# Kernel optimization log

Hardware: AMD Instinct MI355X
Metric: run time of the kernel (lower is better)

The kernel has to match this reference:

```python
import jax, jax.numpy as jnp
import numpy as np

H, D, VD = 8, 64, 64
QD, KD, VDIM, OUT = 512, 512, 512, 512
N, QS, VS = 16, 512, 512
TEMP = 10.0              # softstair_temp
SCALING = D ** -0.5


def _softstair(x):
    fl = jnp.floor(x)
    return fl + jax.nn.sigmoid(TEMP * (jnp.abs(x - fl) - 0.5))


def setup_inputs() -> dict:
    key = jax.random.key(0)
    ks = jax.random.split(key, 24)
    f = jax.random.normal
    s = 0.03  # xavier-ish scale
    return {
        "Q": f(ks[0], (N, QS, QD), jnp.float32),
        "K": f(ks[1], (N, VS, KD), jnp.float32),
        "V": f(ks[2], (N, VS, VDIM), jnp.float32),
        "past_state": f(ks[3], (N, H, QS, D), jnp.float32),
        "past_attention": jax.random.uniform(ks[4], (N, H, QS, 1), jnp.float32),
        "value_positions": jnp.arange(VS, dtype=jnp.float32),
        "attention_mask": jnp.ones((N, QS, VS), jnp.int32),
        "Wq": f(ks[5], (QD, H * D), jnp.float32) * s,
        "Wk": f(ks[6], (KD, H * D), jnp.float32) * s,
        "Wv": f(ks[7], (VDIM, H * VD), jnp.float32) * s,
        "Wpos": f(ks[8], (QD, H * D), jnp.float32) * s,
        "bpos": f(ks[9], (H * D,), jnp.float32) * s,
        "Wsigma": f(ks[10], (H, D, 1), jnp.float32) * s,
        "Wrho": f(ks[11], (H, D, 3), jnp.float32) * s,
        "mix_w": f(ks[12], (QD, 1), jnp.float32) * s,
        "mix_b": f(ks[13], (1,), jnp.float32) * s,
        "gru_wi": f(ks[14], (D, 3 * D), jnp.float32) * s,
        "gru_wh": f(ks[15], (D, 3 * D), jnp.float32) * s,
        "gru_bi": f(ks[16], (3 * D,), jnp.float32) * s,
        "gru_bh": f(ks[17], (3 * D,), jnp.float32) * s,
        "Wc": f(ks[18], (H * VD, OUT), jnp.float32) * s,
    }


def reference(Q, K, V, past_state, past_attention, value_positions, attention_mask,
              Wq, Wk, Wv, Wpos, bpos, Wsigma, Wrho, mix_w, mix_b,
              gru_wi, gru_wh, gru_bi, gru_bh, Wc):
    n, qS, _ = Q.shape
    vS = K.shape[1]
    mask_f = attention_mask.astype(jnp.float32)          # [N,qS,vS]
    mask_b = attention_mask.astype(bool)[:, None]        # [N,1,qS,vS]
    lengths = jnp.sum(mask_f, axis=-1)                   # [N,qS]
    l_1 = jnp.maximum(1.0, lengths - 1.0)[:, None, :, None]
    step_size = 1.0 / l_1                                # [N,1,qS,1]
    nvp = value_positions[None, None, None, :] * step_size  # [N,1,qS,vS]

    # mix gate
    mix = jax.nn.sigmoid(Q @ mix_w + mix_b)[:, None]     # [N,1,qS,1]

    # projections -> [N,H,S,d]
    Qpos = (Q @ Wpos + bpos).reshape(n, qS, H, D).transpose(0, 2, 1, 3)
    Qh = (Q @ Wq).reshape(n, qS, H, D).transpose(0, 2, 1, 3)
    Kh = (K @ Wk).reshape(n, vS, H, D).transpose(0, 2, 1, 3)
    Vh = (V @ Wv).reshape(n, vS, H, VD).transpose(0, 2, 1, 3)

    # content attention
    content = jnp.einsum('bhqd,bhkd->bhqk', Qh, Kh) * SCALING
    content_attn = jax.nn.softmax(jnp.where(mask_b, content, -jnp.inf), axis=-1)

    # GRUCell update (torch gate order r,z,n) on relu(Qpos) with past_state
    x = jax.nn.relu(Qpos)
    gi = x @ gru_wi + gru_bi
    gh = past_state @ gru_wh + gru_bh
    ir, iz, inn = jnp.split(gi, 3, axis=-1)
    hr, hz, hn = jnp.split(gh, 3, axis=-1)
    r = jax.nn.sigmoid(ir + hr)
    z = jax.nn.sigmoid(iz + hz)
    nn_ = jnp.tanh(inn + r * hn)
    state = (1.0 - z) * nn_ + z * past_state             # [N,H,qS,D]

    # location (Gaussian) attention
    sigma = (jax.nn.relu(jnp.einsum('bhqd,hde->bhqe', state, Wsigma)) + 0.27) \
            / lengths[:, None, :, None]                  # [N,H,qS,1]
    rho = jnp.einsum('bhqd,hde->bhqe', state, Wrho)      # [N,H,qS,3]
    steps = _softstair(rho[..., 0:1])
    attn_gate = jax.nn.sigmoid(rho[..., 1:2])
    bias_gate = jax.nn.sigmoid(rho[..., 2:3])
    mu_ = steps * step_size + attn_gate * past_attention + bias_gate
    # leaky clamp to [0,1]
    mu = jnp.maximum(0.01 * mu_, jnp.minimum(mu_, 1.0 + 0.01 * mu_))
    diff = nvp - mu                                      # [N,H,qS,vS]
    gauss = jnp.exp(-(diff * diff) / (2.0 * sigma * sigma))
    g = gauss * mask_f[:, None]
    pos_attn = g / jnp.sum(g + 1e-20, axis=-1, keepdims=True)

    scores = mix * pos_attn + (1.0 - mix) * content_attn
    attended = jnp.einsum('bhqk,bhkv->bhqv', scores, Vh)
    out = attended.transpose(0, 2, 1, 3).reshape(n, qS, H * VD) @ Wc
    return out
```

## Files before the change

kernel.cpp:

```cpp
#include <hip/hip_runtime.h>


typedef __bf16 bf16;
typedef __bf16 bfx8 __attribute__((ext_vector_type(8)));
typedef float v4f __attribute__((ext_vector_type(4)));

__device__ inline float sigm(float x) { return 1.0f / (1.0f + __expf(-x)); }
__device__ inline float tanh_fast(float x) { return 1.0f - 2.0f / (__expf(2.0f * x) + 1.0f); }

__device__ inline v4f mfma16(bfx8 a, bfx8 b, v4f c) {
    return __builtin_amdgcn_mfma_f32_16x16x32_bf16(a, b, c, 0, 0, 0);
}

typedef const __attribute__((address_space(1))) void* gvp;
typedef __attribute__((address_space(3))) void* lvp;

__device__ inline void gload_lds16(const bf16* g, bf16* l) {
    __builtin_amdgcn_global_load_lds((gvp)g, (lvp)l, 16, 0, 0);
}

__device__ inline void split8(const float* __restrict__ p, bfx8& hi, bfx8& lo) {
    float4 x = *(const float4*)p;
    float4 y = *(const float4*)(p + 4);
    float v[8] = {x.x, x.y, x.z, x.w, y.x, y.y, y.z, y.w};
#pragma unroll
    for (int j = 0; j < 8; ++j) {
        bf16 h = (bf16)v[j];
        hi[j] = h;
        lo[j] = (bf16)(v[j] - (float)h);
    }
}

struct PrepArgs {
    const float* wsrc[5]; bf16* wdst[5]; bf16* wdstlo[5];
    const float* gwi; const float* gwh;
    bf16* wih; bf16* wil; bf16* whh; bf16* whl;
    const float* Q; const int* mask; const float* mix_w; const float* mix_b;
    float* mixv; float* stepv; float* lenv; unsigned* mpack;
    const float* Kf; const float* Vf;
    bf16* Qbf; bf16* Qlo; bf16* Kbf; bf16* Vbf;
};

__global__ __launch_bounds__(256) void prep_kernel(PrepArgs a) {
    __shared__ __align__(16) char smraw[17408];
    const int b = blockIdx.x;
    const int t = threadIdx.x;

    if (b < 320) {
        float (*tile)[68] = (float(*)[68])smraw;
        const int wy = b >> 6, bx = b & 63;
        const float* src = a.wsrc[wy];
        bf16* dst = a.wdst[wy];
        bf16* dlo = a.wdstlo[wy];
        const int rbase = (bx >> 3) * 64, cbase = (bx & 7) * 64;
        const int r = t >> 2, cc = (t & 3) * 16;
        {
            const float* p = src + (long)(rbase + r) * 512 + cbase + cc;
            *(float4*)(&tile[r][cc]) = *(const float4*)p;
            *(float4*)(&tile[r][cc + 4]) = *(const float4*)(p + 4);
            *(float4*)(&tile[r][cc + 8]) = *(const float4*)(p + 8);
            *(float4*)(&tile[r][cc + 12]) = *(const float4*)(p + 12);
        }
        __syncthreads();
        bfx8 h0, h1, l0, l1;
#pragma unroll
        for (int j = 0; j < 8; ++j) {
            float v0 = tile[cc + j][r];
            float v1 = tile[cc + 8 + j][r];
            bf16 a0 = (bf16)v0, a1 = (bf16)v1;
            h0[j] = a0; l0[j] = (bf16)(v0 - (float)a0);
            h1[j] = a1; l1[j] = (bf16)(v1 - (float)a1);
        }
        const int n_ = cbase + r;
        const int x_ = (n_ & 7) << 3;
        const long rowo = (long)n_ * 512;
        const int ka = (rbase + cc) ^ x_;
        const int kb = (rbase + cc + 8) ^ x_;
        *(bfx8*)(dst + rowo + ka) = h0;
        *(bfx8*)(dst + rowo + kb) = h1;
        if (dlo) {
            *(bfx8*)(dlo + rowo + ka) = l0;
            *(bfx8*)(dlo + rowo + kb) = l1;
        }
        return;
    }

    if (b < 322) {
        const int m = b - 320;
        const float* src = m ? a.gwh : a.gwi;
        bf16* dh = m ? a.whh : a.wih;
        bf16* dl = m ? a.whl : a.wil;
        for (int e = t; e < 12288; e += 256) {
            int n_ = e >> 6, k = e & 63;
            float v = src[k * 192 + n_];
            bf16 h = (bf16)v;
            dh[e] = h;
            dl[e] = (bf16)(v - (float)h);
        }
        return;
    }

    if (b < 834) {
        unsigned (*mwords)[16] = (unsigned(*)[16])smraw;
        const int bm = b - 322;
        const int qt = bm & 31, n = bm >> 5;
        const int wave = t >> 6, lane = t & 63;
#pragma unroll
        for (int rr = 0; rr < 4; ++rr) {
            const int rloc = wave * 4 + rr;
            const long row = (long)n * 512 + qt * 16 + rloc;
            float dot = 0.f, ms = 0.f;
            unsigned myw = 0;
#pragma unroll
            for (int j = 0; j < 8; ++j) {
                float qv = a.Q[row * 512 + j * 64 + lane];
                float wv = a.mix_w[j * 64 + lane];
                dot += qv * wv;
                int mv = a.mask[row * 512 + j * 64 + lane];
                unsigned long long bl = __ballot(mv != 0);
                ms += (float)__popcll(bl);
                if ((lane >> 1) == j) myw = (unsigned)(bl >> ((lane & 1) * 32));
            }
#pragma unroll
            for (int o = 32; o > 0; o >>= 1) dot += __shfl_xor(dot, o);
            if (lane < 16) mwords[rloc][lane] = myw;
            if (lane == 0) {
                a.mixv[row] = sigm(dot + a.mix_b[0]);
                a.lenv[row] = ms;
                a.stepv[row] = 1.0f / fmaxf(1.0f, ms - 1.0f);
            }
        }
        __syncthreads();
        {
            const int quad = (lane >> 4), c = lane & 15;
            unsigned out = 0;
#pragma unroll
            for (int i = 0; i < 4; ++i) {
                const int rl = quad * 4 + i;
                unsigned w0 = mwords[rl][wave * 4 + 0];
                unsigned w1 = mwords[rl][wave * 4 + 1];
                unsigned w2 = mwords[rl][wave * 4 + 2];
                unsigned w3 = mwords[rl][wave * 4 + 3];
                unsigned byte_ = ((w0 >> c) & 1u) | (((w0 >> (16 + c)) & 1u) << 1) |
                                 (((w1 >> c) & 1u) << 2) | (((w1 >> (16 + c)) & 1u) << 3) |
                                 (((w2 >> c) & 1u) << 4) | (((w2 >> (16 + c)) & 1u) << 5) |
                                 (((w3 >> c) & 1u) << 6) | (((w3 >> (16 + c)) & 1u) << 7);
                out |= byte_ << (8 * i);
            }
            a.mpack[(long)bm * 256 + t] = out;
        }
        return;
    }

    const int cb = b - 834;
    const int tensor = cb >> 10;
    const long off = ((long)(cb & 1023) * 256 + t) * 16;
    const float* s_ = tensor == 0 ? a.Q : (tensor == 1 ? a.Kf : a.Vf);
    const float4* sp = (const float4*)(s_ + off);
    float4 x0 = sp[0], x1 = sp[1], x2 = sp[2], x3 = sp[3];
    float v[16] = {x0.x, x0.y, x0.z, x0.w, x1.x, x1.y, x1.z, x1.w,
                   x2.x, x2.y, x2.z, x2.w, x3.x, x3.y, x3.z, x3.w};
    bfx8 h0, h1, l0, l1;
#pragma unroll
    for (int j = 0; j < 8; ++j) {
        bf16 ha = (bf16)v[j], hb = (bf16)v[8 + j];
        h0[j] = ha; h1[j] = hb;
        l0[j] = (bf16)(v[j] - (float)ha);
        l1[j] = (bf16)(v[8 + j] - (float)hb);
    }
    bf16* dh = tensor == 0 ? a.Qbf : (tensor == 1 ? a.Kbf : a.Vbf);
    *(bfx8*)(dh + off) = h0;
    *(bfx8*)(dh + off + 8) = h1;
    if (tensor == 0) {
        *(bfx8*)(a.Qlo + off) = l0;
        *(bfx8*)(a.Qlo + off + 8) = l1;
    }
}

struct GEMMDesc {
    const bf16* A0;
    const bf16* A1;
    const bf16* B0;
    const bf16* B1;
    const float* bias;
    bf16* Cb;
    bf16* Cl;
    float* Cf;
    int mode;
    float cscale;
};
struct G4 { GEMMDesc d[4]; };

__global__ __launch_bounds__(256, 3) void gemm128(G4 gg) {
    __shared__ bf16 sm[16384];
    bf16* Bs0 = sm;
    bf16* Bs1 = sm + 8192;

    const GEMMDesc g = gg.d[blockIdx.z];
    const int mode = g.mode;
    const int mbase = blockIdx.x * 128, nbase = blockIdx.y * 128;
    const int t = threadIdx.x, w = t >> 6, l = t & 63;
    const int quad = l >> 4, c = l & 15;
    const int wr = w >> 1, wc = w & 1;

    const v4f zero4 = {0.f, 0.f, 0.f, 0.f};
    v4f acc[4][4];
#pragma unroll
    for (int m = 0; m < 4; ++m)
#pragma unroll
        for (int nn = 0; nn < 4; ++nn) acc[m][nn] = zero4;

    const int nsteps = (mode == 2) ? 24 : 8;
    const int xm = c & 7;
    const int slot0 = w * 4;
    const int srow = l >> 3;
    const int sch8 = (l & 7) * 8;
    const long arow = (long)(mbase + wr * 64 + c) * 512 + quad * 8;

    auto issueB = [&](int s, bf16* Bs) {
        const bf16* Bsrc = (mode == 2 && ((s >> 3) == 1)) ? g.B1 : g.B0;
        const int k0 = (mode == 2) ? (s & 7) * 64 : s * 64;
#pragma unroll
        for (int j = 0; j < 4; ++j) {
            int sl = slot0 + j;
            int row = sl * 8 + srow;
            gload_lds16(Bsrc + (long)(nbase + row) * 512 + k0 + sch8, Bs + sl * 512);
        }
    };

    auto loadA = [&](int s, bfx8 (&dst)[8]) {
        const bf16* Asrc = (mode == 2 && ((s >> 3) == 2)) ? g.A1 : g.A0;
        const int k0 = (mode == 2) ? (s & 7) * 64 : s * 64;
#pragma unroll
        for (int m = 0; m < 4; ++m) {
            const bf16* pr = Asrc + arow + (long)m * 16 * 512 + k0;
            dst[m * 2 + 0] = *(const bfx8*)pr;
            dst[m * 2 + 1] = *(const bfx8*)(pr + 32);
        }
    };

    auto computeB = [&](const bf16* Bs, const bfx8 (&af)[8]) {
#pragma unroll
        for (int ks = 0; ks < 2; ++ks) {
            const int off = (((ks * 4 + quad) ^ xm) * 8);
            bfx8 bb[4];
#pragma unroll
            for (int nn = 0; nn < 4; ++nn)
                bb[nn] = *(const bfx8*)(&Bs[(wc * 64 + nn * 16 + c) * 64 + off]);
#pragma unroll
            for (int m = 0; m < 4; ++m)
#pragma unroll
                for (int nn = 0; nn < 4; ++nn)
                    acc[m][nn] = mfma16(af[m * 2 + ks], bb[nn], acc[m][nn]);
        }
    };

    bfx8 aA[8], aB[8];
    issueB(0, Bs0);
    loadA(0, aA);
    __syncthreads();
    for (int s = 0; s < nsteps; s += 2) {
        issueB(s + 1, Bs1);
        loadA(s + 1, aB);
        computeB(Bs0, aA);
        __syncthreads();
        const bool more = (s + 2 < nsteps);
        if (more) {
            issueB(s + 2, Bs0);
            loadA(s + 2, aA);
        }
        computeB(Bs1, aB);
        __syncthreads();
    }

    if (mode == 3) {
        float* C = g.Cf;
#pragma unroll
        for (int m = 0; m < 4; ++m)
#pragma unroll
            for (int nn = 0; nn < 4; ++nn)
#pragma unroll
                for (int i = 0; i < 4; ++i) {
                    int row = mbase + wr * 64 + m * 16 + quad * 4 + i;
                    int col = nbase + wc * 64 + nn * 16 + c;
                    C[(long)row * 512 + col] = acc[m][nn][i];
                }
        return;
    }

    if (mode == 1) {
        bf16* CT = g.Cb + ((long)(mbase >> 9)) * 262144;
        const int s0 = mbase & 511;
        for (int h = 0; h < 2; ++h) {
            if (wr == h) {
#pragma unroll
                for (int m = 0; m < 4; ++m)
#pragma unroll
                    for (int nn = 0; nn < 4; ++nn)
#pragma unroll
                        for (int i = 0; i < 4; ++i)
                            sm[(wc * 64 + nn * 16 + c) * 64 + m * 16 + quad * 4 + i] =
                                (bf16)acc[m][nn][i];
            }
            __syncthreads();
            {
                const bf16* src = sm + (t >> 1) * 64 + (t & 1) * 32;
                bf16* d = CT + (long)(nbase + (t >> 1)) * 512 + s0 + h * 64 + (t & 1) * 32;
#pragma unroll
                for (int j = 0; j < 4; ++j) *(bfx8*)(d + j * 8) = *(const bfx8*)(src + j * 8);
            }
            __syncthreads();
        }
        return;
    }

    for (int h = 0; h < 2; ++h) {
        if (wr == h) {
#pragma unroll
            for (int m = 0; m < 4; ++m)
#pragma unroll
                for (int nn = 0; nn < 4; ++nn)
#pragma unroll
                    for (int i = 0; i < 4; ++i) {
                        int col = wc * 64 + nn * 16 + c;
                        float v = acc[m][nn][i];
                        if (mode == 2) v = fmaxf(v + g.bias[nbase + col], 0.f);
                        else v *= g.cscale;
                        bf16 hv = (bf16)v;
                        sm[(m * 16 + quad * 4 + i) * 128 + col] = hv;
                        if (mode == 2)
                            sm[8192 + (m * 16 + quad * 4 + i) * 128 + col] =
                                (bf16)(v - (float)hv);
                    }
        }
        __syncthreads();
        {
            const int row = t >> 2, seg = t & 3;
            const bf16* src = sm + row * 128 + seg * 32;
            bf16* d = g.Cb + (long)(mbase + h * 64 + row) * 512 + nbase + seg * 32;
#pragma unroll
            for (int j = 0; j < 4; ++j) *(bfx8*)(d + j * 8) = *(const bfx8*)(src + j * 8);
            if (mode == 2) {
                const bf16* src2 = sm + 8192 + row * 128 + seg * 32;
                bf16* d2 = g.Cl + (long)(mbase + h * 64 + row) * 512 + nbase + seg * 32;
#pragma unroll
                for (int j = 0; j < 4; ++j) *(bfx8*)(d2 + j * 8) = *(const bfx8*)(src2 + j * 8);
            }
        }
        __syncthreads();
    }
}

__global__ __launch_bounds__(256) void gru_fused_kernel(
    const bf16* __restrict__ Xh, const bf16* __restrict__ Xl,
    const float* __restrict__ hp,
    const bf16* __restrict__ wih, const bf16* __restrict__ wil,
    const bf16* __restrict__ whh, const bf16* __restrict__ whl,
    const float* __restrict__ gbi, const float* __restrict__ gbh,
    const float* __restrict__ pa, const float* __restrict__ Wsigma,
    const float* __restrict__ Wrho,
    const float* __restrict__ lenv, const float* __restrict__ stepv,
    float* __restrict__ muv, float* __restrict__ sigv) {
    __shared__ bf16 Wh[192][72], Wl[192][72];
    __shared__ float biL[384];

    const int b = blockIdx.x;
    const int qb = b & 7, nh = b >> 3, hd = nh & 7, n = nh >> 3;
    const int t = threadIdx.x;
    const int w = t >> 6, lane = t & 63, quad = lane >> 4, c = lane & 15;
    const int q0 = qb * 64 + w * 16;

    if (t < 192) { biL[t] = gbi[t]; biL[192 + t] = gbh[t]; }
#pragma unroll
    for (int it = 0; it < 6; ++it) {
        int task = it * 256 + t;
        int r = task >> 3, ch = task & 7;
        *(bfx8*)(&Wh[r][ch * 8]) = *(const bfx8*)(wih + r * 64 + ch * 8);
        *(bfx8*)(&Wl[r][ch * 8]) = *(const bfx8*)(wil + r * 64 + ch * 8);
    }
    __syncthreads();

    const v4f zero4 = {0.f, 0.f, 0.f, 0.f};
    v4f gi[12], gh[12];
#pragma unroll
    for (int nt = 0; nt < 12; ++nt) gi[nt] = zero4;
#pragma unroll
    for (int ks = 0; ks < 2; ++ks) {
        long ao = (long)(n * 512 + q0 + c) * 512 + hd * 64 + ks * 32 + quad * 8;
        bfx8 xh = *(const bfx8*)(Xh + ao);
        bfx8 xl = *(const bfx8*)(Xl + ao);
#pragma unroll
        for (int nt = 0; nt < 12; ++nt) {
            bfx8 bh = *(const bfx8*)(&Wh[nt * 16 + c][ks * 32 + quad * 8]);
            bfx8 bl = *(const bfx8*)(&Wl[nt * 16 + c][ks * 32 + quad * 8]);
            gi[nt] = mfma16(xh, bh, gi[nt]);
            gi[nt] = mfma16(xh, bl, gi[nt]);
            gi[nt] = mfma16(xl, bh, gi[nt]);
        }
    }
    __syncthreads();
#pragma unroll
    for (int it = 0; it < 6; ++it) {
        int task = it * 256 + t;
        int r = task >> 3, ch = task & 7;
        *(bfx8*)(&Wh[r][ch * 8]) = *(const bfx8*)(whh + r * 64 + ch * 8);
        *(bfx8*)(&Wl[r][ch * 8]) = *(const bfx8*)(whl + r * 64 + ch * 8);
    }
    __syncthreads();
#pragma unroll
    for (int nt = 0; nt < 12; ++nt) gh[nt] = zero4;
#pragma unroll
    for (int ks = 0; ks < 2; ++ks) {
        bfx8 ah, al;
        split8(hp + (long)(nh * 512 + q0 + c) * 64 + ks * 32 + quad * 8, ah, al);
#pragma unroll
        for (int nt = 0; nt < 12; ++nt) {
            bfx8 bh = *(const bfx8*)(&Wh[nt * 16 + c][ks * 32 + quad * 8]);
            bfx8 bl = *(const bfx8*)(&Wl[nt * 16 + c][ks * 32 + quad * 8]);
            gh[nt] = mfma16(ah, bh, gh[nt]);
            gh[nt] = mfma16(ah, bl, gh[nt]);
            gh[nt] = mfma16(al, bh, gh[nt]);
        }
    }

    float st[4][4];
#pragma unroll
    for (int t4 = 0; t4 < 4; ++t4) {
        float bir = biL[t4 * 16 + c];
        float biz = biL[64 + t4 * 16 + c];
        float bin = biL[128 + t4 * 16 + c];
        float bhr = biL[192 + t4 * 16 + c];
        float bhz = biL[256 + t4 * 16 + c];
        float bhn = biL[320 + t4 * 16 + c];
#pragma unroll
        for (int i = 0; i < 4; ++i) {
            int row = q0 + quad * 4 + i;
            float r = sigm(gi[t4][i] + bir + gh[t4][i] + bhr);
            float z = sigm(gi[t4 + 4][i] + biz + gh[t4 + 4][i] + bhz);
            float nn_ = tanh_fast(gi[t4 + 8][i] + bin + r * (gh[t4 + 8][i] + bhn));
            float hpv = hp[(long)(nh * 512 + row) * 64 + t4 * 16 + c];
            st[t4][i] = (1.0f - z) * nn_ + z * hpv;
        }
    }

    float ws_[4], wr0[4], wr1[4], wr2[4];
#pragma unroll
    for (int t4 = 0; t4 < 4; ++t4) {
        int d = t4 * 16 + c;
        ws_[t4] = Wsigma[hd * 64 + d];
        wr0[t4] = Wrho[(hd * 64 + d) * 3 + 0];
        wr1[t4] = Wrho[(hd * 64 + d) * 3 + 1];
        wr2[t4] = Wrho[(hd * 64 + d) * 3 + 2];
    }
#pragma unroll
    for (int i = 0; i < 4; ++i) {
        float s0 = 0.f, s1 = 0.f, s2 = 0.f, s3 = 0.f;
#pragma unroll
        for (int t4 = 0; t4 < 4; ++t4) {
            float sv = st[t4][i];
            s0 += sv * ws_[t4];
            s1 += sv * wr0[t4];
            s2 += sv * wr1[t4];
            s3 += sv * wr2[t4];
        }
#pragma unroll
        for (int o = 1; o < 16; o <<= 1) {
            s0 += __shfl_xor(s0, o);
            s1 += __shfl_xor(s1, o);
            s2 += __shfl_xor(s2, o);
            s3 += __shfl_xor(s3, o);
        }
        if (c == 0) {
            int row = q0 + quad * 4 + i;
            int idx = nh * 512 + row, rq = n * 512 + row;
            float L = lenv[rq], sp = stepv[rq];
            float sg = (fmaxf(s0, 0.f) + 0.27f) / L;
            float fl = floorf(s1);
            float steps = fl + sigm(10.0f * (fabsf(s1 - fl) - 0.5f));
            float ag = sigm(s2), bg = sigm(s3);
            float mu_ = steps * sp + ag * pa[idx] + bg;
            float mu = fmaxf(0.01f * mu_, fminf(mu_, 1.0f + 0.01f * mu_));
            muv[idx] = mu;
            sigv[idx] = sg;
        }
    }
}

__global__ __launch_bounds__(256) void attn_fused_kernel(
    const bf16* __restrict__ Qh, const bf16* __restrict__ Kh,
    const bf16* __restrict__ VhT, const unsigned* __restrict__ mpack,
    const float* __restrict__ vpos, const float* __restrict__ mixv,
    const float* __restrict__ stepv, const float* __restrict__ muv,
    const float* __restrict__ sigv, bf16* __restrict__ att) {
    __shared__ bf16 Pp[16][520];
    __shared__ bf16 Pg[16][520];

    const int b = blockIdx.x;
    const int nh = ((b >> 8) << 3) | (b & 7);
    const int qt = (b >> 3) & 31;
    const int hd = nh & 7, n = nh >> 3;
    const int t = threadIdx.x;
    const int wave = t >> 6, lane = t & 63;
    const int quad = lane >> 4, c = lane & 15;
    const int qloc = quad * 4;

    const bf16* qrow = Qh + (long)(n * 512 + qt * 16 + c) * 512 + hd * 64 + quad * 8;
    bfx8 afr0 = *(const bfx8*)qrow;
    bfx8 afr1 = *(const bfx8*)(qrow + 32);

    const v4f zero4 = {0.f, 0.f, 0.f, 0.f};
    v4f acc[8];
#pragma unroll
    for (int i = 0; i < 8; ++i) acc[i] = zero4;

    const bf16* kbase = Kh + (long)(n * 512 + wave * 128 + c) * 512 + hd * 64 + quad * 8;
#pragma unroll
    for (int t8 = 0; t8 < 8; ++t8) {
        bfx8 b0 = *(const bfx8*)(kbase + (long)t8 * 16 * 512);
        bfx8 b1 = *(const bfx8*)(kbase + (long)t8 * 16 * 512 + 32);
        acc[t8] = mfma16(afr0, b0, acc[t8]);
        acc[t8] = mfma16(afr1, b1, acc[t8]);
    }

    float mu_[4], c2n[4], stp[4];
#pragma unroll
    for (int i = 0; i < 4; ++i) {
        int q = qt * 16 + qloc + i;
        int idx = nh * 512 + q, rq = n * 512 + q;
        mu_[i] = muv[idx];
        float sg = sigv[idx];
        c2n[i] = -0.72134752f / (sg * sg);
        stp[i] = stepv[rq];
    }

    const unsigned mb32 = mpack[(long)(n * 32 + qt) * 256 + t];
    unsigned mbits[4];
#pragma unroll
    for (int i = 0; i < 4; ++i) mbits[i] = (mb32 >> (8 * i)) & 0xffu;

    float vp[8];
#pragma unroll
    for (int t8 = 0; t8 < 8; ++t8) vp[t8] = vpos[wave * 128 + t8 * 16 + c];

#pragma unroll
    for (int i = 0; i < 4; ++i) {
        float m = mu_[i], s = stp[i], cg = c2n[i];
#pragma unroll
        for (int t8 = 0; t8 < 8; ++t8) {
            int on = (mbits[i] >> t8) & 1;
            float pv = on ? __builtin_amdgcn_exp2f(acc[t8][i]) : 0.f;
            float d = vp[t8] * s - m;
            float gv = on ? __builtin_amdgcn_exp2f(d * d * cg) : 0.f;
            int k = wave * 128 + t8 * 16 + c;
            Pp[qloc + i][k] = (bf16)pv;
            Pg[qloc + i][k] = (bf16)gv;
        }
    }

    __syncthreads();

    bfx8 ones;
#pragma unroll
    for (int j = 0; j < 8; ++j) ones[j] = (bf16)1.0f;

    v4f accP = zero4, accG = zero4, accS = zero4, accT = zero4;
    const bf16* vrow = VhT + (long)(n * 512 + hd * 64 + wave * 16 + c) * 512 + quad * 8;
    __builtin_amdgcn_s_setprio(1);
#pragma unroll
    for (int ks = 0; ks < 16; ++ks) {
        bfx8 bf_ = *(const bfx8*)(vrow + ks * 32);
        bfx8 ap = *(const bfx8*)(&Pp[c][ks * 32 + quad * 8]);
        bfx8 ag = *(const bfx8*)(&Pg[c][ks * 32 + quad * 8]);
        accP = mfma16(ap, bf_, accP);
        accG = mfma16(ag, bf_, accG);
        accS = mfma16(ap, ones, accS);
        accT = mfma16(ag, ones, accT);
    }
    __builtin_amdgcn_s_setprio(0);

#pragma unroll
    for (int i = 0; i < 4; ++i) {
        float Sp = accS[i];
        float Sg = accT[i] + 512.0f * 1e-20f;
        float m_ = mixv[n * 512 + qt * 16 + qloc + i];
        float aci = (1.0f - m_) / Sp;
        float bci = m_ / Sg;
        int q = qt * 16 + quad * 4 + i;
        att[(long)(n * 512 + q) * 512 + hd * 64 + wave * 16 + c] =
            (bf16)(aci * accP[i] + bci * accG[i]);
    }
}

extern "C" void kernel_launch(void* const* d_in, const int* in_sizes, int n_in,
                              void* d_out, int out_size, void* d_ws, size_t ws_size,
                              hipStream_t stream) {
    (void)in_sizes; (void)n_in; (void)out_size; (void)ws_size;

    const float* Q = (const float*)d_in[0];
    const float* K = (const float*)d_in[1];
    const float* V = (const float*)d_in[2];
    const float* past_state = (const float*)d_in[3];
    const float* past_att = (const float*)d_in[4];
    const float* vpos = (const float*)d_in[5];
    const int* mask = (const int*)d_in[6];
    const float* Wq = (const float*)d_in[7];
    const float* Wk = (const float*)d_in[8];
    const float* Wv = (const float*)d_in[9];
    const float* Wpos = (const float*)d_in[10];
    const float* bpos = (const float*)d_in[11];
    const float* Wsigma = (const float*)d_in[12];
    const float* Wrho = (const float*)d_in[13];
    const float* mix_w = (const float*)d_in[14];
    const float* mix_b = (const float*)d_in[15];
    const float* gwi = (const float*)d_in[16];
    const float* gwh = (const float*)d_in[17];
    const float* gbi = (const float*)d_in[18];
    const float* gbh = (const float*)d_in[19];
    const float* Wc = (const float*)d_in[20];
    float* out = (float*)d_out;

    char* p = (char*)d_ws;
    const size_t SZB = 8192UL * 512 * 2;
    const size_t SZW = 512UL * 512 * 2;
    bf16* WqT = (bf16*)p;   p += SZW;
    bf16* WkT = (bf16*)p;   p += SZW;
    bf16* WvT = (bf16*)p;   p += SZW;
    bf16* WpT = (bf16*)p;   p += SZW;
    bf16* WpTl = (bf16*)p;  p += SZW;
    bf16* WcT = (bf16*)p;   p += SZW;
    bf16* wih = (bf16*)p;   p += 24576;
    bf16* wil = (bf16*)p;   p += 24576;
    bf16* whh = (bf16*)p;   p += 24576;
    bf16* whl = (bf16*)p;   p += 24576;
    bf16* Qh = (bf16*)p;    p += SZB;
    bf16* Kh = (bf16*)p;    p += SZB;
    bf16* VhT = (bf16*)p;   p += SZB;
    bf16* Xh = (bf16*)p;
    bf16* att = Xh;         p += SZB;
    bf16* Xl = (bf16*)p;    p += SZB;
    bf16* Qbf = (bf16*)p;   p += SZB;
    bf16* Qlo = (bf16*)p;   p += SZB;
    bf16* Kbf = (bf16*)p;   p += SZB;
    bf16* Vbf = (bf16*)p;   p += SZB;
    unsigned* mpack = (unsigned*)p;      p += 16UL * 32 * 256 * 4;
    float* mixv = (float*)p;  p += 32768;
    float* stepv = (float*)p; p += 32768;
    float* lenv = (float*)p;  p += 32768;
    float* muv = (float*)p;   p += 262144;
    float* sigv = (float*)p;  p += 262144;

    dim3 blk(256);

    PrepArgs pa;
    pa.wsrc[0] = Wq; pa.wsrc[1] = Wk; pa.wsrc[2] = Wv; pa.wsrc[3] = Wpos; pa.wsrc[4] = Wc;
    pa.wdst[0] = WqT; pa.wdst[1] = WkT; pa.wdst[2] = WvT; pa.wdst[3] = WpT; pa.wdst[4] = WcT;
    pa.wdstlo[0] = nullptr; pa.wdstlo[1] = nullptr; pa.wdstlo[2] = nullptr;
    pa.wdstlo[3] = WpTl; pa.wdstlo[4] = nullptr;
    pa.gwi = gwi; pa.gwh = gwh;
    pa.wih = wih; pa.wil = wil; pa.whh = whh; pa.whl = whl;
    pa.Q = Q; pa.mask = mask; pa.mix_w = mix_w; pa.mix_b = mix_b;
    pa.mixv = mixv; pa.stepv = stepv; pa.lenv = lenv; pa.mpack = mpack;
    pa.Kf = K; pa.Vf = V;
    pa.Qbf = Qbf; pa.Qlo = Qlo; pa.Kbf = Kbf; pa.Vbf = Vbf;
    prep_kernel<<<dim3(3906), blk, 0, stream>>>(pa);

    G4 gp;
    gp.d[0].A0 = Qbf; gp.d[0].A1 = Qlo; gp.d[0].B0 = WpT; gp.d[0].B1 = WpTl;
    gp.d[0].bias = bpos; gp.d[0].Cb = Xh; gp.d[0].Cl = Xl; gp.d[0].Cf = nullptr;
    gp.d[0].mode = 2; gp.d[0].cscale = 1.0f;
    gp.d[1].A0 = Qbf; gp.d[1].A1 = nullptr; gp.d[1].B0 = WqT; gp.d[1].B1 = nullptr;
    gp.d[1].bias = nullptr; gp.d[1].Cb = Qh; gp.d[1].Cl = nullptr; gp.d[1].Cf = nullptr;
    gp.d[1].mode = 0; gp.d[1].cscale = 0.125f * 1.44269504089f;
    gp.d[2].A0 = Kbf; gp.d[2].A1 = nullptr; gp.d[2].B0 = WkT; gp.d[2].B1 = nullptr;
    gp.d[2].bias = nullptr; gp.d[2].Cb = Kh; gp.d[2].Cl = nullptr; gp.d[2].Cf = nullptr;
    gp.d[2].mode = 0; gp.d[2].cscale = 1.0f;
    gp.d[3].A0 = Vbf; gp.d[3].A1 = nullptr; gp.d[3].B0 = WvT; gp.d[3].B1 = nullptr;
    gp.d[3].bias = nullptr; gp.d[3].Cb = VhT; gp.d[3].Cl = nullptr; gp.d[3].Cf = nullptr;
    gp.d[3].mode = 1; gp.d[3].cscale = 1.0f;
    gemm128<<<dim3(64, 4, 4), blk, 0, stream>>>(gp);

    gru_fused_kernel<<<dim3(1024), blk, 0, stream>>>(
        Xh, Xl, past_state, wih, wil, whh, whl, gbi, gbh, past_att, Wsigma, Wrho,
        lenv, stepv, muv, sigv);

    attn_fused_kernel<<<dim3(4096), blk, 0, stream>>>(
        Qh, Kh, VhT, mpack, vpos, mixv, stepv, muv, sigv, att);

    G4 go;
    go.d[0].A0 = att; go.d[0].A1 = nullptr; go.d[0].B0 = WcT; go.d[0].B1 = nullptr;
    go.d[0].bias = nullptr; go.d[0].Cb = nullptr; go.d[0].Cl = nullptr; go.d[0].Cf = out;
    go.d[0].mode = 3; go.d[0].cscale = 1.0f;
    go.d[1] = go.d[0]; go.d[2] = go.d[0]; go.d[3] = go.d[0];
    gemm128<<<dim3(64, 4, 1), blk, 0, stream>>>(go);
}
```

Baseline: 370.0 us.

## Fuse fp32-to-bf16 activation conversion into projection GEMM A-tile staging

Removes the separate prep pass that converted Q, K and V to bf16 (plus Q's low-part split) and the extra intermediate buffers. The GEMM now reads fp32 activations directly, converts them in registers, and writes them into a swizzled LDS A tile. K-steps shrink from 64 to 32 so both A and B fit in the double buffer. The LDS swizzles for the weights and the attention output change to match the new 32-wide tile layout. This saves global round-trip traffic and a lot of prep blocks, at the cost of more K-loop iterations, more barriers and conversion ALU work inside the GEMM.

```diff
diff --git a/kernel.cpp b/kernel.cpp
--- a/kernel.cpp
+++ b/kernel.cpp
@@ -37,8 +37,6 @@
     bf16* wih; bf16* wil; bf16* whh; bf16* whl;
     const float* Q; const int* mask; const float* mix_w; const float* mix_b;
     float* mixv; float* stepv; float* lenv; unsigned* mpack;
-    const float* Kf; const float* Vf;
-    bf16* Qbf; bf16* Qlo; bf16* Kbf; bf16* Vbf;
 };
 
 __global__ __launch_bounds__(256) void prep_kernel(PrepArgs a) {
@@ -72,7 +70,7 @@
             h1[j] = a1; l1[j] = (bf16)(v1 - (float)a1);
         }
         const int n_ = cbase + r;
-        const int x_ = (n_ & 7) << 3;
+        const int x_ = (n_ & 3) << 3;
         const long rowo = (long)n_ * 512;
         const int ka = (rbase + cc) ^ x_;
         const int kb = (rbase + cc + 8) ^ x_;
@@ -100,86 +98,59 @@
         return;
     }
 
-    if (b < 834) {
-        unsigned (*mwords)[16] = (unsigned(*)[16])smraw;
-        const int bm = b - 322;
-        const int qt = bm & 31, n = bm >> 5;
-        const int wave = t >> 6, lane = t & 63;
-#pragma unroll
-        for (int rr = 0; rr < 4; ++rr) {
-            const int rloc = wave * 4 + rr;
-            const long row = (long)n * 512 + qt * 16 + rloc;
-            float dot = 0.f, ms = 0.f;
-            unsigned myw = 0;
-#pragma unroll
-            for (int j = 0; j < 8; ++j) {
-                float qv = a.Q[row * 512 + j * 64 + lane];
-                float wv = a.mix_w[j * 64 + lane];
-                dot += qv * wv;
-                int mv = a.mask[row * 512 + j * 64 + lane];
-                unsigned long long bl = __ballot(mv != 0);
-                ms += (float)__popcll(bl);
-                if ((lane >> 1) == j) myw = (unsigned)(bl >> ((lane & 1) * 32));
-            }
-#pragma unroll
-            for (int o = 32; o > 0; o >>= 1) dot += __shfl_xor(dot, o);
-            if (lane < 16) mwords[rloc][lane] = myw;
-            if (lane == 0) {
-                a.mixv[row] = sigm(dot + a.mix_b[0]);
-                a.lenv[row] = ms;
-                a.stepv[row] = 1.0f / fmaxf(1.0f, ms - 1.0f);
-            }
-        }
-        __syncthreads();
-        {
-            const int quad = (lane >> 4), c = lane & 15;
-            unsigned out = 0;
-#pragma unroll
-            for (int i = 0; i < 4; ++i) {
-                const int rl = quad * 4 + i;
-                unsigned w0 = mwords[rl][wave * 4 + 0];
-                unsigned w1 = mwords[rl][wave * 4 + 1];
-                unsigned w2 = mwords[rl][wave * 4 + 2];
-                unsigned w3 = mwords[rl][wave * 4 + 3];
-                unsigned byte_ = ((w0 >> c) & 1u) | (((w0 >> (16 + c)) & 1u) << 1) |
-                                 (((w1 >> c) & 1u) << 2) | (((w1 >> (16 + c)) & 1u) << 3) |
-                                 (((w2 >> c) & 1u) << 4) | (((w2 >> (16 + c)) & 1u) << 5) |
-                                 (((w3 >> c) & 1u) << 6) | (((w3 >> (16 + c)) & 1u) << 7);
-                out |= byte_ << (8 * i);
-            }
-            a.mpack[(long)bm * 256 + t] = out;
-        }
-        return;
-    }
-
-    const int cb = b - 834;
-    const int tensor = cb >> 10;
-    const long off = ((long)(cb & 1023) * 256 + t) * 16;
-    const float* s_ = tensor == 0 ? a.Q : (tensor == 1 ? a.Kf : a.Vf);
-    const float4* sp = (const float4*)(s_ + off);
-    float4 x0 = sp[0], x1 = sp[1], x2 = sp[2], x3 = sp[3];
-    float v[16] = {x0.x, x0.y, x0.z, x0.w, x1.x, x1.y, x1.z, x1.w,
-                   x2.x, x2.y, x2.z, x2.w, x3.x, x3.y, x3.z, x3.w};
-    bfx8 h0, h1, l0, l1;
-#pragma unroll
-    for (int j = 0; j < 8; ++j) {
-        bf16 ha = (bf16)v[j], hb = (bf16)v[8 + j];
-        h0[j] = ha; h1[j] = hb;
-        l0[j] = (bf16)(v[j] - (float)ha);
-        l1[j] = (bf16)(v[8 + j] - (float)hb);
-    }
-    bf16* dh = tensor == 0 ? a.Qbf : (tensor == 1 ? a.Kbf : a.Vbf);
-    *(bfx8*)(dh + off) = h0;
-    *(bfx8*)(dh + off + 8) = h1;
-    if (tensor == 0) {
-        *(bfx8*)(a.Qlo + off) = l0;
-        *(bfx8*)(a.Qlo + off + 8) = l1;
+    unsigned (*mwords)[16] = (unsigned(*)[16])smraw;
+    const int bm = b - 322;
+    const int qt = bm & 31, n = bm >> 5;
+    const int wave = t >> 6, lane = t & 63;
+#pragma unroll
+    for (int rr = 0; rr < 4; ++rr) {
+        const int rloc = wave * 4 + rr;
+        const long row = (long)n * 512 + qt * 16 + rloc;
+        float dot = 0.f, ms = 0.f;
+        unsigned myw = 0;
+#pragma unroll
+        for (int j = 0; j < 8; ++j) {
+            float qv = a.Q[row * 512 + j * 64 + lane];
+            float wv = a.mix_w[j * 64 + lane];
+            dot += qv * wv;
+            int mv = a.mask[row * 512 + j * 64 + lane];
+            unsigned long long bl = __ballot(mv != 0);
+            ms += (float)__popcll(bl);
+            if ((lane >> 1) == j) myw = (unsigned)(bl >> ((lane & 1) * 32));
+        }
+#pragma unroll
+        for (int o = 32; o > 0; o >>= 1) dot += __shfl_xor(dot, o);
+        if (lane < 16) mwords[rloc][lane] = myw;
+        if (lane == 0) {
+            a.mixv[row] = sigm(dot + a.mix_b[0]);
+            a.lenv[row] = ms;
+            a.stepv[row] = 1.0f / fmaxf(1.0f, ms - 1.0f);
+        }
+    }
+    __syncthreads();
+    {
+        const int quad = (lane >> 4), c = lane & 15;
+        unsigned out = 0;
+#pragma unroll
+        for (int i = 0; i < 4; ++i) {
+            const int rl = quad * 4 + i;
+            unsigned w0 = mwords[rl][wave * 4 + 0];
+            unsigned w1 = mwords[rl][wave * 4 + 1];
+            unsigned w2 = mwords[rl][wave * 4 + 2];
+            unsigned w3 = mwords[rl][wave * 4 + 3];
+            unsigned byte_ = ((w0 >> c) & 1u) | (((w0 >> (16 + c)) & 1u) << 1) |
+                             (((w1 >> c) & 1u) << 2) | (((w1 >> (16 + c)) & 1u) << 3) |
+                             (((w2 >> c) & 1u) << 4) | (((w2 >> (16 + c)) & 1u) << 5) |
+                             (((w3 >> c) & 1u) << 6) | (((w3 >> (16 + c)) & 1u) << 7);
+            out |= byte_ << (8 * i);
+        }
+        a.mpack[(long)bm * 256 + t] = out;
     }
 }
 
 struct GEMMDesc {
-    const bf16* A0;
-    const bf16* A1;
+    const float* Af;
+    const bf16* Ab;
     const bf16* B0;
     const bf16* B1;
     const float* bias;
@@ -193,8 +164,6 @@
 
 __global__ __launch_bounds__(256, 3) void gemm128(G4 gg) {
     __shared__ bf16 sm[16384];
-    bf16* Bs0 = sm;
-    bf16* Bs1 = sm + 8192;
 
     const GEMMDesc g = gg.d[blockIdx.z];
     const int mode = g.mode;
@@ -210,66 +179,93 @@
 #pragma unroll
         for (int nn = 0; nn < 4; ++nn) acc[m][nn] = zero4;
 
-    const int nsteps = (mode == 2) ? 24 : 8;
-    const int xm = c & 7;
-    const int slot0 = w * 4;
-    const int srow = l >> 3;
-    const int sch8 = (l & 7) * 8;
-    const long arow = (long)(mbase + wr * 64 + c) * 512 + quad * 8;
-
-    auto issueB = [&](int s, bf16* Bs) {
-        const bf16* Bsrc = (mode == 2 && ((s >> 3) == 1)) ? g.B1 : g.B0;
-        const int k0 = (mode == 2) ? (s & 7) * 64 : s * 64;
-#pragma unroll
-        for (int j = 0; j < 4; ++j) {
-            int sl = slot0 + j;
-            int row = sl * 8 + srow;
-            gload_lds16(Bsrc + (long)(nbase + row) * 512 + k0 + sch8, Bs + sl * 512);
+    const int nsteps = (mode == 2) ? 48 : 16;
+    const int off = ((quad ^ (c & 3)) << 3);
+    const int arw = t >> 1;
+    const int ach = t & 1;
+    const int brow = l >> 2, bch8 = (l & 3) * 8;
+
+    float4 aA[4], aB[4];
+
+    auto issue = [&](int s, bf16* As, bf16* Bs, float4 (&ar)[4]) {
+        const bf16* Bsrc = (mode == 2 && ((s >> 4) == 1)) ? g.B1 : g.B0;
+        const int k0 = (mode == 2) ? (s & 15) * 32 : s * 32;
+#pragma unroll
+        for (int j = 0; j < 2; ++j) {
+            int rg = (w * 2 + j) * 16;
+            gload_lds16(Bsrc + (long)(nbase + rg + brow) * 512 + k0 + bch8,
+                        Bs + rg * 32);
+        }
+        if (mode == 3) {
+#pragma unroll
+            for (int j = 0; j < 2; ++j) {
+                int rg = (w * 2 + j) * 16;
+                gload_lds16(g.Ab + (long)(mbase + rg + brow) * 512 + k0 + bch8,
+                            As + rg * 32);
+            }
+        } else {
+            const float* p = g.Af + (long)(mbase + arw) * 512 + k0 + ach * 16;
+            ar[0] = *(const float4*)p;
+            ar[1] = *(const float4*)(p + 4);
+            ar[2] = *(const float4*)(p + 8);
+            ar[3] = *(const float4*)(p + 12);
         }
     };
 
-    auto loadA = [&](int s, bfx8 (&dst)[8]) {
-        const bf16* Asrc = (mode == 2 && ((s >> 3) == 2)) ? g.A1 : g.A0;
-        const int k0 = (mode == 2) ? (s & 7) * 64 : s * 64;
-#pragma unroll
-        for (int m = 0; m < 4; ++m) {
-            const bf16* pr = Asrc + arow + (long)m * 16 * 512 + k0;
-            dst[m * 2 + 0] = *(const bfx8*)pr;
-            dst[m * 2 + 1] = *(const bfx8*)(pr + 32);
+    auto writeA = [&](int s, bf16* As, const float4 (&ar)[4]) {
+        if (mode == 3) return;
+        const bool lo = (mode == 2) && ((s >> 4) == 2);
+        float v[16] = {ar[0].x, ar[0].y, ar[0].z, ar[0].w,
+                       ar[1].x, ar[1].y, ar[1].z, ar[1].w,
+                       ar[2].x, ar[2].y, ar[2].z, ar[2].w,
+                       ar[3].x, ar[3].y, ar[3].z, ar[3].w};
+#pragma unroll
+        for (int u = 0; u < 2; ++u) {
+            bfx8 hv;
+            if (!lo) {
+#pragma unroll
+                for (int q = 0; q < 8; ++q) hv[q] = (bf16)v[u * 8 + q];
+            } else {
+#pragma unroll
+                for (int q = 0; q < 8; ++q) {
+                    bf16 h = (bf16)v[u * 8 + q];
+                    hv[q] = (bf16)(v[u * 8 + q] - (float)h);
+                }
+            }
+            const int ch = (ach * 2 + u) ^ (arw & 3);
+            *(bfx8*)(&As[arw * 32 + ch * 8]) = hv;
         }
     };
 
-    auto computeB = [&](const bf16* Bs, const bfx8 (&af)[8]) {
-#pragma unroll
-        for (int ks = 0; ks < 2; ++ks) {
-            const int off = (((ks * 4 + quad) ^ xm) * 8);
-            bfx8 bb[4];
+    auto compute = [&](const bf16* As, const bf16* Bs) {
+        bfx8 af[4], bb[4];
+#pragma unroll
+        for (int m = 0; m < 4; ++m)
+            af[m] = *(const bfx8*)(&As[(wr * 64 + m * 16 + c) * 32 + off]);
+#pragma unroll
+        for (int nn = 0; nn < 4; ++nn)
+            bb[nn] = *(const bfx8*)(&Bs[(wc * 64 + nn * 16 + c) * 32 + off]);
+#pragma unroll
+        for (int m = 0; m < 4; ++m)
 #pragma unroll
             for (int nn = 0; nn < 4; ++nn)
-                bb[nn] = *(const bfx8*)(&Bs[(wc * 64 + nn * 16 + c) * 64 + off]);
-#pragma unroll
-            for (int m = 0; m < 4; ++m)
-#pragma unroll
-                for (int nn = 0; nn < 4; ++nn)
-                    acc[m][nn] = mfma16(af[m * 2 + ks], bb[nn], acc[m][nn]);
-        }
+                acc[m][nn] = mfma16(af[m], bb[nn], acc[m][nn]);
     };
 
-    bfx8 aA[8], aB[8];
-    issueB(0, Bs0);
-    loadA(0, aA);
+    bf16* buf0 = sm;
+    bf16* buf1 = sm + 8192;
+    issue(0, buf0, buf0 + 4096, aA);
+    writeA(0, buf0, aA);
     __syncthreads();
     for (int s = 0; s < nsteps; s += 2) {
-        issueB(s + 1, Bs1);
-        loadA(s + 1, aB);
-        computeB(Bs0, aA);
+        issue(s + 1, buf1, buf1 + 4096, aB);
+        compute(buf0, buf0 + 4096);
+        writeA(s + 1, buf1, aB);
         __syncthreads();
         const bool more = (s + 2 < nsteps);
-        if (more) {
-            issueB(s + 2, Bs0);
-            loadA(s + 2, aA);
-        }
-        computeB(Bs1, aB);
+        if (more) issue(s + 2, buf0, buf0 + 4096, aA);
+        compute(buf1, buf1 + 4096);
+        if (more) writeA(s + 2, buf0, aA);
         __syncthreads();
     }
 
@@ -586,7 +582,8 @@
         float aci = (1.0f - m_) / Sp;
         float bci = m_ / Sg;
         int q = qt * 16 + quad * 4 + i;
-        att[(long)(n * 512 + q) * 512 + hd * 64 + wave * 16 + c] =
+        int cx = (wave * 16 + c) ^ (i << 3);
+        att[(long)(n * 512 + q) * 512 + hd * 64 + cx] =
             (bf16)(aci * accP[i] + bci * accG[i]);
     }
 }
@@ -638,10 +635,6 @@
     bf16* Xh = (bf16*)p;
     bf16* att = Xh;         p += SZB;
     bf16* Xl = (bf16*)p;    p += SZB;
-    bf16* Qbf = (bf16*)p;   p += SZB;
-    bf16* Qlo = (bf16*)p;   p += SZB;
-    bf16* Kbf = (bf16*)p;   p += SZB;
-    bf16* Vbf = (bf16*)p;   p += SZB;
     unsigned* mpack = (unsigned*)p;      p += 16UL * 32 * 256 * 4;
     float* mixv = (float*)p;  p += 32768;
     float* stepv = (float*)p; p += 32768;
@@ -660,21 +653,19 @@
     pa.wih = wih; pa.wil = wil; pa.whh = whh; pa.whl = whl;
     pa.Q = Q; pa.mask = mask; pa.mix_w = mix_w; pa.mix_b = mix_b;
     pa.mixv = mixv; pa.stepv = stepv; pa.lenv = lenv; pa.mpack = mpack;
-    pa.Kf = K; pa.Vf = V;
-    pa.Qbf = Qbf; pa.Qlo = Qlo; pa.Kbf = Kbf; pa.Vbf = Vbf;
-    prep_kernel<<<dim3(3906), blk, 0, stream>>>(pa);
+    prep_kernel<<<dim3(834), blk, 0, stream>>>(pa);
 
     G4 gp;
-    gp.d[0].A0 = Qbf; gp.d[0].A1 = Qlo; gp.d[0].B0 = WpT; gp.d[0].B1 = WpTl;
+    gp.d[0].Af = Q;  gp.d[0].Ab = nullptr; gp.d[0].B0 = WpT; gp.d[0].B1 = WpTl;
     gp.d[0].bias = bpos; gp.d[0].Cb = Xh; gp.d[0].Cl = Xl; gp.d[0].Cf = nullptr;
     gp.d[0].mode = 2; gp.d[0].cscale = 1.0f;
-    gp.d[1].A0 = Qbf; gp.d[1].A1 = nullptr; gp.d[1].B0 = WqT; gp.d[1].B1 = nullptr;
+    gp.d[1].Af = Q;  gp.d[1].Ab = nullptr; gp.d[1].B0 = WqT; gp.d[1].B1 = nullptr;
     gp.d[1].bias = nullptr; gp.d[1].Cb = Qh; gp.d[1].Cl = nullptr; gp.d[1].Cf = nullptr;
     gp.d[1].mode = 0; gp.d[1].cscale = 0.125f * 1.44269504089f;
-    gp.d[2].A0 = Kbf; gp.d[2].A1 = nullptr; gp.d[2].B0 = WkT; gp.d[2].B1 = nullptr;
+    gp.d[2].Af = K;  gp.d[2].Ab = nullptr; gp.d[2].B0 = WkT; gp.d[2].B1 = nullptr;
     gp.d[2].bias = nullptr; gp.d[2].Cb = Kh; gp.d[2].Cl = nullptr; gp.d[2].Cf = nullptr;
     gp.d[2].mode = 0; gp.d[2].cscale = 1.0f;
-    gp.d[3].A0 = Vbf; gp.d[3].A1 = nullptr; gp.d[3].B0 = WvT; gp.d[3].B1 = nullptr;
+    gp.d[3].Af = V;  gp.d[3].Ab = nullptr; gp.d[3].B0 = WvT; gp.d[3].B1 = nullptr;
     gp.d[3].bias = nullptr; gp.d[3].Cb = VhT; gp.d[3].Cl = nullptr; gp.d[3].Cf = nullptr;
     gp.d[3].mode = 1; gp.d[3].cscale = 1.0f;
     gemm128<<<dim3(64, 4, 4), blk, 0, stream>>>(gp);
@@ -687,7 +678,7 @@
         Qh, Kh, VhT, mpack, vpos, mixv, stepv, muv, sigv, att);
 
     G4 go;
-    go.d[0].A0 = att; go.d[0].A1 = nullptr; go.d[0].B0 = WcT; go.d[0].B1 = nullptr;
+    go.d[0].Af = nullptr; go.d[0].Ab = att; go.d[0].B0 = WcT; go.d[0].B1 = nullptr;
     go.d[0].bias = nullptr; go.d[0].Cb = nullptr; go.d[0].Cl = nullptr; go.d[0].Cf = out;
     go.d[0].mode = 3; go.d[0].cscale = 1.0f;
     go.d[1] = go.d[0]; go.d[2] = go.d[0]; go.d[3] = go.d[0];
```

Measured after the change: 340.8 us. 1.09x faster.
